# Performance work log

Hardware: AMD Instinct MI355X
Metric: run time of the kernel (lower is better)

## Reference

```python
import jax, jax.numpy as jnp
import numpy as np

B, H, S, D = 8, 16, 1024, 64

def setup_inputs() -> dict:
    key = jax.random.key(0)
    k1, k2, k3, k4 = jax.random.split(key, 4)
    Q = jax.random.normal(k1, (B, H, S, D), dtype=jnp.float32)
    K = jax.random.normal(k2, (B, H, S, D), dtype=jnp.float32)
    V = jax.random.normal(k3, (B, H, S, D), dtype=jnp.float32)
    mask = jax.random.randint(k4, (B,), 0, 2).astype(jnp.bool_)
    return {"Q": Q, "K": K, "V": V, "mask": mask}

def reference(Q, K, V, mask):
    # scores: [B,H,S,S]
    scores = jnp.einsum('bhqd,bhkd->bhqk', Q, K)
    # per-batch-element mask broadcast over heads and both seq dims
    scores = jnp.where(mask[:, None, None, None], jnp.float32(-1e9), scores)
    # NOTE: original divides by sqrt(d) AFTER masking, so masked value is -1e9/sqrt(d)
    inv_sqrt_d = jnp.float32(1.0 / np.sqrt(Q.shape[-1]))
    attn = jax.nn.softmax(scores * inv_sqrt_d, axis=-1)
    return jnp.einsum('bhqk,bhkd->bhqd', attn, V)
```

## Files before the change

### kernel.cpp

```cpp
#include <hip/hip_runtime.h>
#include <hip/hip_bf16.h>

typedef __bf16 bf16;
typedef __bf16 bf16x4 __attribute__((ext_vector_type(4)));
typedef __bf16 bf16x8 __attribute__((ext_vector_type(8)));
typedef float  f32x16 __attribute__((ext_vector_type(16)));

#define S_  1024
#define D_  64
#define BQ  256
#define BK  64
#define KT  (S_/BK)
#define QT  (S_/BQ)
#define LD  72

#define ZERO16 {0.f,0.f,0.f,0.f,0.f,0.f,0.f,0.f,0.f,0.f,0.f,0.f,0.f,0.f,0.f,0.f}

__global__ __launch_bounds__(256, 2)
void fa_fwd(const float* __restrict__ Q, const float* __restrict__ K,
            const float* __restrict__ V, const int* __restrict__ mask,
            float* __restrict__ O)
{
    __shared__ bf16 ks[2][BK][LD];
    __shared__ bf16 vt[2][D_][LD];

    const int tid  = threadIdx.x;
    const int lane = tid & 63;
    const int w    = tid >> 6;
    const int l32  = lane & 31;
    const int hi   = lane >> 5;
    const int bid  = blockIdx.x;

    int um[8] = { mask[0] == 0, mask[1] == 0, mask[2] == 0, mask[3] == 0,
                  mask[4] == 0, mask[5] == 0, mask[6] == 0, mask[7] == 0 };
    int U = 0;
    #pragma unroll
    for (int i = 0; i < 8; ++i) U += um[i];
    const int nHeavy = 64 * U;
    const int nLight = 16 * (8 - U);

    int bh, qtile;
    bool light;
    if (bid < nHeavy) {
        const int xcd = bid & 7;
        const int r   = bid >> 3;
        qtile = r & 3;
        const int g   = r >> 2;
        const int bh_rank = (g << 3) | xcd;
        const int ub   = bh_rank >> 4;
        const int head = bh_rank & 15;
        int b = 0, cnt = 0;
        #pragma unroll
        for (int i = 0; i < 8; ++i) { if (um[i]) { if (cnt == ub) b = i; ++cnt; } }
        bh = b * 16 + head;
        light = false;
    } else if (bid < nHeavy + nLight) {
        const int lid    = bid - nHeavy;
        const int m_rank = lid >> 4;
        const int head   = lid & 15;
        int b = 0, cnt = 0;
        #pragma unroll
        for (int i = 0; i < 8; ++i) { if (!um[i]) { if (cnt == m_rank) b = i; ++cnt; } }
        bh = b * 16 + head;
        qtile = 0;
        light = true;
    } else {
        return;
    }

    const size_t base = (size_t)bh * (S_ * D_);

    if (light) {
        const float4* gvl = (const float4*)(V + base);
        float4*       gol = (float4*)(O + base);
        const int d4 = tid & 15;
        const int rg = tid >> 4;
        float4 acc = {0.f, 0.f, 0.f, 0.f};
        #pragma unroll 4
        for (int r = 0; r < 64; ++r) {
            float4 v = gvl[(rg * 64 + r) * 16 + d4];
            acc.x += v.x; acc.y += v.y; acc.z += v.z; acc.w += v.w;
        }
        float4 (*red)[16] = (float4(*)[16])&ks[0][0][0];
        red[rg][d4] = acc;
        __syncthreads();
        if (tid < 16) {
            float4 s = red[0][tid];
            #pragma unroll
            for (int g = 1; g < 16; ++g) {
                float4 t = red[g][tid];
                s.x += t.x; s.y += t.y; s.z += t.z; s.w += t.w;
            }
            const float sc = 1.0f / 1024.0f;
            s.x *= sc; s.y *= sc; s.z *= sc; s.w *= sc;
            red[0][tid] = s;
        }
        __syncthreads();
        float4 mv = red[0][d4];
        #pragma unroll 4
        for (int k = 0; k < 64; ++k)
            gol[(rg + 16 * k) * 16 + d4] = mv;
        return;
    }

    const int qW = qtile * BQ + w * 64;
    const float qscale = 0.1803368801111204f;

    const int vkq = (tid >> 2) & 15;
    const int vkp = (vkq & 12) | ((vkq & 1) << 1) | ((vkq >> 1) & 1);
    const int vc4 = (tid & 3) + 4 * w;
    const float4* gk = (const float4*)(K + base);
    const float4* gv = (const float4*)(V + base);

    float4 kr[4], vr[4];
    #pragma unroll
    for (int it = 0; it < 4; ++it) kr[it] = gk[it * 256 + tid];
    #pragma unroll
    for (int r = 0; r < 4; ++r)    vr[r]  = gv[(vkq * 4 + r) * 16 + vc4];

    bf16x8 qf[2][4];
    #pragma unroll
    for (int nt = 0; nt < 2; ++nt) {
        const float* qp = Q + base + (size_t)(qW + nt * 32 + l32) * D_ + hi * 8;
        #pragma unroll
        for (int kc = 0; kc < 4; ++kc) {
            float4 a = *(const float4*)(qp + kc * 16);
            float4 c = *(const float4*)(qp + kc * 16 + 4);
            bf16x8 f;
            f[0] = (bf16)(a.x * qscale); f[1] = (bf16)(a.y * qscale);
            f[2] = (bf16)(a.z * qscale); f[3] = (bf16)(a.w * qscale);
            f[4] = (bf16)(c.x * qscale); f[5] = (bf16)(c.y * qscale);
            f[6] = (bf16)(c.z * qscale); f[7] = (bf16)(c.w * qscale);
            qf[nt][kc] = f;
        }
    }

    f32x16 o[2][2];
    #pragma unroll
    for (int dm = 0; dm < 2; ++dm)
        #pragma unroll
        for (int nt = 0; nt < 2; ++nt) o[dm][nt] = (f32x16)ZERO16;
    float lsum[2] = {0.f, 0.f};

    auto mkpf = [&](const f32x16& sv, bf16x8& fA, bf16x8& fB, float& ls) {
        bf16x8 a, c;
        #pragma unroll
        for (int i = 0; i < 8; ++i) {
            float e0 = __builtin_amdgcn_exp2f(sv[i]);
            float e1 = __builtin_amdgcn_exp2f(sv[8 + i]);
            ls += e0 + e1;
            a[i] = (bf16)e0;
            c[i] = (bf16)e1;
        }
        fA = a; fB = c;
    };

    for (int kt = 0; kt < KT; ++kt) {
        bf16 (*ksb)[LD] = ks[kt & 1];
        bf16 (*vtb)[LD] = vt[kt & 1];

        #pragma unroll
        for (int it = 0; it < 4; ++it) {
            int i = it * 256 + tid;
            int row = i >> 4, c4 = i & 15;
            bf16x4 hk = {(bf16)kr[it].x, (bf16)kr[it].y, (bf16)kr[it].z, (bf16)kr[it].w};
            *(bf16x4*)&ksb[row][c4 * 4] = hk;
        }
        {
            bf16x4 t0 = {(bf16)vr[0].x, (bf16)vr[1].x, (bf16)vr[2].x, (bf16)vr[3].x};
            bf16x4 t1 = {(bf16)vr[0].y, (bf16)vr[1].y, (bf16)vr[2].y, (bf16)vr[3].y};
            bf16x4 t2 = {(bf16)vr[0].z, (bf16)vr[1].z, (bf16)vr[2].z, (bf16)vr[3].z};
            bf16x4 t3 = {(bf16)vr[0].w, (bf16)vr[1].w, (bf16)vr[2].w, (bf16)vr[3].w};
            *(bf16x4*)&vtb[vc4 * 4 + 0][vkp * 4] = t0;
            *(bf16x4*)&vtb[vc4 * 4 + 1][vkp * 4] = t1;
            *(bf16x4*)&vtb[vc4 * 4 + 2][vkp * 4] = t2;
            *(bf16x4*)&vtb[vc4 * 4 + 3][vkp * 4] = t3;
        }

        __syncthreads();

        {
            int ktn = (kt + 1 < KT) ? (kt + 1) : kt;
            #pragma unroll
            for (int it = 0; it < 4; ++it) kr[it] = gk[ktn * 1024 + it * 256 + tid];
            #pragma unroll
            for (int r = 0; r < 4; ++r)    vr[r]  = gv[ktn * 1024 + (vkq * 4 + r) * 16 + vc4];
        }

        f32x16 s00 = ZERO16, s01 = ZERO16, s10 = ZERO16, s11 = ZERO16;
        #pragma unroll
        for (int kc = 0; kc < 4; ++kc) {
            bf16x8 k0 = *(const bf16x8*)&ksb[l32][kc * 16 + hi * 8];
            bf16x8 k1 = *(const bf16x8*)&ksb[32 + l32][kc * 16 + hi * 8];
            s00 = __builtin_amdgcn_mfma_f32_32x32x16_bf16(k0, qf[0][kc], s00, 0, 0, 0);
            s01 = __builtin_amdgcn_mfma_f32_32x32x16_bf16(k0, qf[1][kc], s01, 0, 0, 0);
            s10 = __builtin_amdgcn_mfma_f32_32x32x16_bf16(k1, qf[0][kc], s10, 0, 0, 0);
            s11 = __builtin_amdgcn_mfma_f32_32x32x16_bf16(k1, qf[1][kc], s11, 0, 0, 0);
        }

        bf16x8 pf[4][2];
        mkpf(s00, pf[0][0], pf[1][0], lsum[0]);
        mkpf(s01, pf[0][1], pf[1][1], lsum[1]);
        mkpf(s10, pf[2][0], pf[3][0], lsum[0]);
        mkpf(s11, pf[2][1], pf[3][1], lsum[1]);

        #pragma unroll
        for (int kc = 0; kc < 4; ++kc) {
            bf16x8 v0 = *(const bf16x8*)&vtb[l32][kc * 16 + hi * 8];
            bf16x8 v1 = *(const bf16x8*)&vtb[32 + l32][kc * 16 + hi * 8];
            o[0][0] = __builtin_amdgcn_mfma_f32_32x32x16_bf16(v0, pf[kc][0], o[0][0], 0, 0, 0);
            o[0][1] = __builtin_amdgcn_mfma_f32_32x32x16_bf16(v0, pf[kc][1], o[0][1], 0, 0, 0);
            o[1][0] = __builtin_amdgcn_mfma_f32_32x32x16_bf16(v1, pf[kc][0], o[1][0], 0, 0, 0);
            o[1][1] = __builtin_amdgcn_mfma_f32_32x32x16_bf16(v1, pf[kc][1], o[1][1], 0, 0, 0);
        }
    }

    #pragma unroll
    for (int nt = 0; nt < 2; ++nt) {
        float lv = lsum[nt] + __shfl_xor(lsum[nt], 32);
        float inv = 1.0f / lv;
        float* op = O + base + (size_t)(qW + nt * 32 + l32) * D_ + hi * 4;
        #pragma unroll
        for (int g = 0; g < 4; ++g) {
            float4 a = { o[0][nt][g * 4 + 0] * inv, o[0][nt][g * 4 + 1] * inv,
                         o[0][nt][g * 4 + 2] * inv, o[0][nt][g * 4 + 3] * inv };
            *(float4*)(op + g * 8) = a;
            float4 c = { o[1][nt][g * 4 + 0] * inv, o[1][nt][g * 4 + 1] * inv,
                         o[1][nt][g * 4 + 2] * inv, o[1][nt][g * 4 + 3] * inv };
            *(float4*)(op + 32 + g * 8) = c;
        }
    }
}

extern "C" void kernel_launch(void* const* d_in, const int* in_sizes, int n_in,
                              void* d_out, int out_size, void* d_ws, size_t ws_size,
                              hipStream_t stream)
{
    const float* Q    = (const float*)d_in[0];
    const float* K    = (const float*)d_in[1];
    const float* V    = (const float*)d_in[2];
    const int*   mask = (const int*)d_in[3];
    float*       O    = (float*)d_out;

    dim3 grid(8 * 16 * QT);
    fa_fwd<<<grid, 256, 0, stream>>>(Q, K, V, mask, O);
}
```

Before: 142.1 us.

## Software-pipeline QK and PV halves across key tiles with triple-buffered LDS

Splits each key tile's QK^T and exp/PV work into two 32-row halves and interleaves them across iterations, so the exp of one half overlaps MFMA work from the other half and the previous tile. LDS K/V buffers go from double to triple so the previous tile's V stays valid while the next tile is staged. The aim is to hide the exp2 and conversion latency behind matrix-core work. In exchange it uses more shared memory, which may reduce occupancy, and keeps more score accumulators live, which raises register pressure.

```diff
diff --git a/kernel.cpp b/kernel.cpp
--- a/kernel.cpp
+++ b/kernel.cpp
@@ -21,8 +21,8 @@
             const float* __restrict__ V, const int* __restrict__ mask,
             float* __restrict__ O)
 {
-    __shared__ bf16 ks[2][BK][LD];
-    __shared__ bf16 vt[2][D_][LD];
+    __shared__ bf16 ks[3][BK][LD];
+    __shared__ bf16 vt[3][D_][LD];
 
     const int tid  = threadIdx.x;
     const int lane = tid & 63;
@@ -142,6 +142,42 @@
         for (int nt = 0; nt < 2; ++nt) o[dm][nt] = (f32x16)ZERO16;
     float lsum[2] = {0.f, 0.f};
 
+    auto stage_to = [&](int bsel) {
+        bf16 (*ksb)[LD] = ks[bsel];
+        bf16 (*vtb)[LD] = vt[bsel];
+        #pragma unroll
+        for (int it = 0; it < 4; ++it) {
+            int i = it * 256 + tid;
+            int row = i >> 4, c4 = i & 15;
+            bf16x4 hk = {(bf16)kr[it].x, (bf16)kr[it].y, (bf16)kr[it].z, (bf16)kr[it].w};
+            *(bf16x4*)&ksb[row][c4 * 4] = hk;
+        }
+        bf16x4 t0 = {(bf16)vr[0].x, (bf16)vr[1].x, (bf16)vr[2].x, (bf16)vr[3].x};
+        bf16x4 t1 = {(bf16)vr[0].y, (bf16)vr[1].y, (bf16)vr[2].y, (bf16)vr[3].y};
+        bf16x4 t2 = {(bf16)vr[0].z, (bf16)vr[1].z, (bf16)vr[2].z, (bf16)vr[3].z};
+        bf16x4 t3 = {(bf16)vr[0].w, (bf16)vr[1].w, (bf16)vr[2].w, (bf16)vr[3].w};
+        *(bf16x4*)&vtb[vc4 * 4 + 0][vkp * 4] = t0;
+        *(bf16x4*)&vtb[vc4 * 4 + 1][vkp * 4] = t1;
+        *(bf16x4*)&vtb[vc4 * 4 + 2][vkp * 4] = t2;
+        *(bf16x4*)&vtb[vc4 * 4 + 3][vkp * 4] = t3;
+    };
+    auto prefetch_t = [&](int t) {
+        #pragma unroll
+        for (int it = 0; it < 4; ++it) kr[it] = gk[t * 1024 + it * 256 + tid];
+        #pragma unroll
+        for (int r = 0; r < 4; ++r)    vr[r]  = gv[t * 1024 + (vkq * 4 + r) * 16 + vc4];
+    };
+
+    auto qk_half = [&](int bsel, int rowoff, f32x16& s_0, f32x16& s_1) {
+        bf16 (*ksb)[LD] = ks[bsel];
+        #pragma unroll
+        for (int kc = 0; kc < 4; ++kc) {
+            bf16x8 kf = *(const bf16x8*)&ksb[rowoff + l32][kc * 16 + hi * 8];
+            s_0 = __builtin_amdgcn_mfma_f32_32x32x16_bf16(kf, qf[0][kc], s_0, 0, 0, 0);
+            s_1 = __builtin_amdgcn_mfma_f32_32x32x16_bf16(kf, qf[1][kc], s_1, 0, 0, 0);
+        }
+    };
+
     auto mkpf = [&](const f32x16& sv, bf16x8& fA, bf16x8& fB, float& ls) {
         bf16x8 a, c;
         #pragma unroll
@@ -155,65 +191,50 @@
         fA = a; fB = c;
     };
 
-    for (int kt = 0; kt < KT; ++kt) {
-        bf16 (*ksb)[LD] = ks[kt & 1];
-        bf16 (*vtb)[LD] = vt[kt & 1];
-
-        #pragma unroll
-        for (int it = 0; it < 4; ++it) {
-            int i = it * 256 + tid;
-            int row = i >> 4, c4 = i & 15;
-            bf16x4 hk = {(bf16)kr[it].x, (bf16)kr[it].y, (bf16)kr[it].z, (bf16)kr[it].w};
-            *(bf16x4*)&ksb[row][c4 * 4] = hk;
-        }
-        {
-            bf16x4 t0 = {(bf16)vr[0].x, (bf16)vr[1].x, (bf16)vr[2].x, (bf16)vr[3].x};
-            bf16x4 t1 = {(bf16)vr[0].y, (bf16)vr[1].y, (bf16)vr[2].y, (bf16)vr[3].y};
-            bf16x4 t2 = {(bf16)vr[0].z, (bf16)vr[1].z, (bf16)vr[2].z, (bf16)vr[3].z};
-            bf16x4 t3 = {(bf16)vr[0].w, (bf16)vr[1].w, (bf16)vr[2].w, (bf16)vr[3].w};
-            *(bf16x4*)&vtb[vc4 * 4 + 0][vkp * 4] = t0;
-            *(bf16x4*)&vtb[vc4 * 4 + 1][vkp * 4] = t1;
-            *(bf16x4*)&vtb[vc4 * 4 + 2][vkp * 4] = t2;
-            *(bf16x4*)&vtb[vc4 * 4 + 3][vkp * 4] = t3;
-        }
-
+    auto exp_pv_half = [&](const f32x16& s_0, const f32x16& s_1, int bsel, int kc0) {
+        bf16x8 a0, a1, b0, b1;
+        mkpf(s_0, a0, b0, lsum[0]);
+        mkpf(s_1, a1, b1, lsum[1]);
+        bf16 (*vtb)[LD] = vt[bsel];
+        bf16x8 v0 = *(const bf16x8*)&vtb[l32][kc0 * 16 + hi * 8];
+        bf16x8 v1 = *(const bf16x8*)&vtb[32 + l32][kc0 * 16 + hi * 8];
+        o[0][0] = __builtin_amdgcn_mfma_f32_32x32x16_bf16(v0, a0, o[0][0], 0, 0, 0);
+        o[0][1] = __builtin_amdgcn_mfma_f32_32x32x16_bf16(v0, a1, o[0][1], 0, 0, 0);
+        o[1][0] = __builtin_amdgcn_mfma_f32_32x32x16_bf16(v1, a0, o[1][0], 0, 0, 0);
+        o[1][1] = __builtin_amdgcn_mfma_f32_32x32x16_bf16(v1, a1, o[1][1], 0, 0, 0);
+        bf16x8 w0 = *(const bf16x8*)&vtb[l32][(kc0 + 1) * 16 + hi * 8];
+        bf16x8 w1 = *(const bf16x8*)&vtb[32 + l32][(kc0 + 1) * 16 + hi * 8];
+        o[0][0] = __builtin_amdgcn_mfma_f32_32x32x16_bf16(w0, b0, o[0][0], 0, 0, 0);
+        o[0][1] = __builtin_amdgcn_mfma_f32_32x32x16_bf16(w0, b1, o[0][1], 0, 0, 0);
+        o[1][0] = __builtin_amdgcn_mfma_f32_32x32x16_bf16(w1, b0, o[1][0], 0, 0, 0);
+        o[1][1] = __builtin_amdgcn_mfma_f32_32x32x16_bf16(w1, b1, o[1][1], 0, 0, 0);
+    };
+
+    f32x16 sA0, sA1, sB0, sB1;
+
+    stage_to(0);
+    __syncthreads();
+    prefetch_t(1);
+    sA0 = (f32x16)ZERO16; sA1 = (f32x16)ZERO16;
+    qk_half(0, 0,  sA0, sA1);
+    sB0 = (f32x16)ZERO16; sB1 = (f32x16)ZERO16;
+    qk_half(0, 32, sB0, sB1);
+    exp_pv_half(sA0, sA1, 0, 0);
+
+    int bs = 1, bp = 0;
+    for (int kt = 1; kt < KT; ++kt) {
+        stage_to(bs);
         __syncthreads();
-
-        {
-            int ktn = (kt + 1 < KT) ? (kt + 1) : kt;
-            #pragma unroll
-            for (int it = 0; it < 4; ++it) kr[it] = gk[ktn * 1024 + it * 256 + tid];
-            #pragma unroll
-            for (int r = 0; r < 4; ++r)    vr[r]  = gv[ktn * 1024 + (vkq * 4 + r) * 16 + vc4];
-        }
-
-        f32x16 s00 = ZERO16, s01 = ZERO16, s10 = ZERO16, s11 = ZERO16;
-        #pragma unroll
-        for (int kc = 0; kc < 4; ++kc) {
-            bf16x8 k0 = *(const bf16x8*)&ksb[l32][kc * 16 + hi * 8];
-            bf16x8 k1 = *(const bf16x8*)&ksb[32 + l32][kc * 16 + hi * 8];
-            s00 = __builtin_amdgcn_mfma_f32_32x32x16_bf16(k0, qf[0][kc], s00, 0, 0, 0);
-            s01 = __builtin_amdgcn_mfma_f32_32x32x16_bf16(k0, qf[1][kc], s01, 0, 0, 0);
-            s10 = __builtin_amdgcn_mfma_f32_32x32x16_bf16(k1, qf[0][kc], s10, 0, 0, 0);
-            s11 = __builtin_amdgcn_mfma_f32_32x32x16_bf16(k1, qf[1][kc], s11, 0, 0, 0);
-        }
-
-        bf16x8 pf[4][2];
-        mkpf(s00, pf[0][0], pf[1][0], lsum[0]);
-        mkpf(s01, pf[0][1], pf[1][1], lsum[1]);
-        mkpf(s10, pf[2][0], pf[3][0], lsum[0]);
-        mkpf(s11, pf[2][1], pf[3][1], lsum[1]);
-
-        #pragma unroll
-        for (int kc = 0; kc < 4; ++kc) {
-            bf16x8 v0 = *(const bf16x8*)&vtb[l32][kc * 16 + hi * 8];
-            bf16x8 v1 = *(const bf16x8*)&vtb[32 + l32][kc * 16 + hi * 8];
-            o[0][0] = __builtin_amdgcn_mfma_f32_32x32x16_bf16(v0, pf[kc][0], o[0][0], 0, 0, 0);
-            o[0][1] = __builtin_amdgcn_mfma_f32_32x32x16_bf16(v0, pf[kc][1], o[0][1], 0, 0, 0);
-            o[1][0] = __builtin_amdgcn_mfma_f32_32x32x16_bf16(v1, pf[kc][0], o[1][0], 0, 0, 0);
-            o[1][1] = __builtin_amdgcn_mfma_f32_32x32x16_bf16(v1, pf[kc][1], o[1][1], 0, 0, 0);
-        }
-    }
+        prefetch_t((kt + 1 < KT) ? (kt + 1) : kt);
+        sA0 = (f32x16)ZERO16; sA1 = (f32x16)ZERO16;
+        qk_half(bs, 0, sA0, sA1);
+        exp_pv_half(sB0, sB1, bp, 2);
+        sB0 = (f32x16)ZERO16; sB1 = (f32x16)ZERO16;
+        qk_half(bs, 32, sB0, sB1);
+        exp_pv_half(sA0, sA1, bs, 0);
+        bp = bs; bs = (bs == 2) ? 0 : bs + 1;
+    }
+    exp_pv_half(sB0, sB1, bp, 2);
 
     #pragma unroll
     for (int nt = 0; nt < 2; ++nt) {
```

New measurement: 145.3 us. 1.02x slower.

## Split block into producer and consumer wavefronts for K/V staging

Applied to the files above, without the earlier changes.

The block grows to 512 threads. Four new producer wavefronts load K/V from global memory, convert them to bf16 and stage them into double-buffered LDS, while the original four wavefronts only run the MFMA attention loop. The aim is to take global-load latency and conversion work off the compute wavefronts. The cost is a larger block, with launch bounds of 512x2 that squeeze the register budget per thread, which may cause spills in the consumer path. The light mean path is re-indexed for 512 threads.

```diff
diff --git a/kernel.cpp b/kernel.cpp
--- a/kernel.cpp
+++ b/kernel.cpp
@@ -16,7 +16,7 @@
 
 #define ZERO16 {0.f,0.f,0.f,0.f,0.f,0.f,0.f,0.f,0.f,0.f,0.f,0.f,0.f,0.f,0.f,0.f}
 
-__global__ __launch_bounds__(256, 2)
+__global__ __launch_bounds__(512, 2)
 void fa_fwd(const float* __restrict__ Q, const float* __restrict__ K,
             const float* __restrict__ V, const int* __restrict__ mask,
             float* __restrict__ O)
@@ -77,8 +77,8 @@
         const int rg = tid >> 4;
         float4 acc = {0.f, 0.f, 0.f, 0.f};
         #pragma unroll 4
-        for (int r = 0; r < 64; ++r) {
-            float4 v = gvl[(rg * 64 + r) * 16 + d4];
+        for (int r = 0; r < 32; ++r) {
+            float4 v = gvl[(rg * 32 + r) * 16 + d4];
             acc.x += v.x; acc.y += v.y; acc.z += v.z; acc.w += v.w;
         }
         float4 (*red)[16] = (float4(*)[16])&ks[0][0][0];
@@ -87,7 +87,7 @@
         if (tid < 16) {
             float4 s = red[0][tid];
             #pragma unroll
-            for (int g = 1; g < 16; ++g) {
+            for (int g = 1; g < 32; ++g) {
                 float4 t = red[g][tid];
                 s.x += t.x; s.y += t.y; s.z += t.z; s.w += t.w;
             }
@@ -98,136 +98,151 @@
         __syncthreads();
         float4 mv = red[0][d4];
         #pragma unroll 4
-        for (int k = 0; k < 64; ++k)
-            gol[(rg + 16 * k) * 16 + d4] = mv;
+        for (int k = 0; k < 32; ++k)
+            gol[(rg + 32 * k) * 16 + d4] = mv;
         return;
     }
 
-    const int qW = qtile * BQ + w * 64;
+    const bool consumer = (w < 4);
     const float qscale = 0.1803368801111204f;
 
-    const int vkq = (tid >> 2) & 15;
-    const int vkp = (vkq & 12) | ((vkq & 1) << 1) | ((vkq >> 1) & 1);
-    const int vc4 = (tid & 3) + 4 * w;
-    const float4* gk = (const float4*)(K + base);
-    const float4* gv = (const float4*)(V + base);
-
-    float4 kr[4], vr[4];
-    #pragma unroll
-    for (int it = 0; it < 4; ++it) kr[it] = gk[it * 256 + tid];
-    #pragma unroll
-    for (int r = 0; r < 4; ++r)    vr[r]  = gv[(vkq * 4 + r) * 16 + vc4];
-
-    bf16x8 qf[2][4];
-    #pragma unroll
-    for (int nt = 0; nt < 2; ++nt) {
-        const float* qp = Q + base + (size_t)(qW + nt * 32 + l32) * D_ + hi * 8;
-        #pragma unroll
-        for (int kc = 0; kc < 4; ++kc) {
-            float4 a = *(const float4*)(qp + kc * 16);
-            float4 c = *(const float4*)(qp + kc * 16 + 4);
-            bf16x8 f;
-            f[0] = (bf16)(a.x * qscale); f[1] = (bf16)(a.y * qscale);
-            f[2] = (bf16)(a.z * qscale); f[3] = (bf16)(a.w * qscale);
-            f[4] = (bf16)(c.x * qscale); f[5] = (bf16)(c.y * qscale);
-            f[6] = (bf16)(c.z * qscale); f[7] = (bf16)(c.w * qscale);
-            qf[nt][kc] = f;
-        }
-    }
-
-    f32x16 o[2][2];
-    #pragma unroll
-    for (int dm = 0; dm < 2; ++dm)
-        #pragma unroll
-        for (int nt = 0; nt < 2; ++nt) o[dm][nt] = (f32x16)ZERO16;
-    float lsum[2] = {0.f, 0.f};
-
-    auto mkpf = [&](const f32x16& sv, bf16x8& fA, bf16x8& fB, float& ls) {
-        bf16x8 a, c;
-        #pragma unroll
-        for (int i = 0; i < 8; ++i) {
-            float e0 = __builtin_amdgcn_exp2f(sv[i]);
-            float e1 = __builtin_amdgcn_exp2f(sv[8 + i]);
-            ls += e0 + e1;
-            a[i] = (bf16)e0;
-            c[i] = (bf16)e1;
-        }
-        fA = a; fB = c;
-    };
-
-    for (int kt = 0; kt < KT; ++kt) {
-        bf16 (*ksb)[LD] = ks[kt & 1];
-        bf16 (*vtb)[LD] = vt[kt & 1];
-
-        #pragma unroll
-        for (int it = 0; it < 4; ++it) {
-            int i = it * 256 + tid;
-            int row = i >> 4, c4 = i & 15;
-            bf16x4 hk = {(bf16)kr[it].x, (bf16)kr[it].y, (bf16)kr[it].z, (bf16)kr[it].w};
-            *(bf16x4*)&ksb[row][c4 * 4] = hk;
-        }
-        {
+    if (consumer) {
+        const int qW = qtile * BQ + w * 64;
+
+        bf16x8 qf[2][4];
+        #pragma unroll
+        for (int nt = 0; nt < 2; ++nt) {
+            const float* qp = Q + base + (size_t)(qW + nt * 32 + l32) * D_ + hi * 8;
+            #pragma unroll
+            for (int kc = 0; kc < 4; ++kc) {
+                float4 a = *(const float4*)(qp + kc * 16);
+                float4 c = *(const float4*)(qp + kc * 16 + 4);
+                bf16x8 f;
+                f[0] = (bf16)(a.x * qscale); f[1] = (bf16)(a.y * qscale);
+                f[2] = (bf16)(a.z * qscale); f[3] = (bf16)(a.w * qscale);
+                f[4] = (bf16)(c.x * qscale); f[5] = (bf16)(c.y * qscale);
+                f[6] = (bf16)(c.z * qscale); f[7] = (bf16)(c.w * qscale);
+                qf[nt][kc] = f;
+            }
+        }
+
+        f32x16 o[2][2];
+        #pragma unroll
+        for (int dm = 0; dm < 2; ++dm)
+            #pragma unroll
+            for (int nt = 0; nt < 2; ++nt) o[dm][nt] = (f32x16)ZERO16;
+        float lsum[2] = {0.f, 0.f};
+
+        auto mkpf = [&](const f32x16& sv, bf16x8& fA, bf16x8& fB, float& ls) {
+            bf16x8 a, c;
+            #pragma unroll
+            for (int i = 0; i < 8; ++i) {
+                float e0 = __builtin_amdgcn_exp2f(sv[i]);
+                float e1 = __builtin_amdgcn_exp2f(sv[8 + i]);
+                ls += e0 + e1;
+                a[i] = (bf16)e0;
+                c[i] = (bf16)e1;
+            }
+            fA = a; fB = c;
+        };
+
+        __syncthreads();
+
+        for (int kt = 0; kt < KT; ++kt) {
+            bf16 (*ksb)[LD] = ks[kt & 1];
+            bf16 (*vtb)[LD] = vt[kt & 1];
+
+            f32x16 s00 = ZERO16, s01 = ZERO16, s10 = ZERO16, s11 = ZERO16;
+            #pragma unroll
+            for (int kc = 0; kc < 4; ++kc) {
+                bf16x8 k0 = *(const bf16x8*)&ksb[l32][kc * 16 + hi * 8];
+                bf16x8 k1 = *(const bf16x8*)&ksb[32 + l32][kc * 16 + hi * 8];
+                s00 = __builtin_amdgcn_mfma_f32_32x32x16_bf16(k0, qf[0][kc], s00, 0, 0, 0);
+                s01 = __builtin_amdgcn_mfma_f32_32x32x16_bf16(k0, qf[1][kc], s01, 0, 0, 0);
+                s10 = __builtin_amdgcn_mfma_f32_32x32x16_bf16(k1, qf[0][kc], s10, 0, 0, 0);
+                s11 = __builtin_amdgcn_mfma_f32_32x32x16_bf16(k1, qf[1][kc], s11, 0, 0, 0);
+            }
+
+            bf16x8 pf[4][2];
+            mkpf(s00, pf[0][0], pf[1][0], lsum[0]);
+            mkpf(s01, pf[0][1], pf[1][1], lsum[1]);
+            mkpf(s10, pf[2][0], pf[3][0], lsum[0]);
+            mkpf(s11, pf[2][1], pf[3][1], lsum[1]);
+
+            #pragma unroll
+            for (int kc = 0; kc < 4; ++kc) {
+                bf16x8 v0 = *(const bf16x8*)&vtb[l32][kc * 16 + hi * 8];
+                bf16x8 v1 = *(const bf16x8*)&vtb[32 + l32][kc * 16 + hi * 8];
+                o[0][0] = __builtin_amdgcn_mfma_f32_32x32x16_bf16(v0, pf[kc][0], o[0][0], 0, 0, 0);
+                o[0][1] = __builtin_amdgcn_mfma_f32_32x32x16_bf16(v0, pf[kc][1], o[0][1], 0, 0, 0);
+                o[1][0] = __builtin_amdgcn_mfma_f32_32x32x16_bf16(v1, pf[kc][0], o[1][0], 0, 0, 0);
+                o[1][1] = __builtin_amdgcn_mfma_f32_32x32x16_bf16(v1, pf[kc][1], o[1][1], 0, 0, 0);
+            }
+
+            __syncthreads();
+        }
+
+        #pragma unroll
+        for (int nt = 0; nt < 2; ++nt) {
+            float lv = lsum[nt] + __shfl_xor(lsum[nt], 32);
+            float inv = 1.0f / lv;
+            float* op = O + base + (size_t)(qW + nt * 32 + l32) * D_ + hi * 4;
+            #pragma unroll
+            for (int g = 0; g < 4; ++g) {
+                float4 a = { o[0][nt][g * 4 + 0] * inv, o[0][nt][g * 4 + 1] * inv,
+                             o[0][nt][g * 4 + 2] * inv, o[0][nt][g * 4 + 3] * inv };
+                *(float4*)(op + g * 8) = a;
+                float4 c = { o[1][nt][g * 4 + 0] * inv, o[1][nt][g * 4 + 1] * inv,
+                             o[1][nt][g * 4 + 2] * inv, o[1][nt][g * 4 + 3] * inv };
+                *(float4*)(op + 32 + g * 8) = c;
+            }
+        }
+    } else {
+        const int t2  = tid - 256;
+        const int vkq = (t2 >> 2) & 15;
+        const int vkp = (vkq & 12) | ((vkq & 1) << 1) | ((vkq >> 1) & 1);
+        const int vc4 = (t2 & 3) + 4 * ((t2 >> 6) & 3);
+        const float4* gk = (const float4*)(K + base);
+        const float4* gv = (const float4*)(V + base);
+
+        float4 kr[4], vr[4];
+        auto prefetch_t = [&](int t) {
+            #pragma unroll
+            for (int it = 0; it < 4; ++it) kr[it] = gk[t * 1024 + it * 256 + t2];
+            #pragma unroll
+            for (int r = 0; r < 4; ++r)    vr[r]  = gv[t * 1024 + (vkq * 4 + r) * 16 + vc4];
+        };
+        auto stage_to = [&](int bsel) {
+            bf16 (*ksb)[LD] = ks[bsel];
+            bf16 (*vtb)[LD] = vt[bsel];
+            #pragma unroll
+            for (int it = 0; it < 4; ++it) {
+                int i = it * 256 + t2;
+                int row = i >> 4, c4 = i & 15;
+                bf16x4 hk = {(bf16)kr[it].x, (bf16)kr[it].y, (bf16)kr[it].z, (bf16)kr[it].w};
+                *(bf16x4*)&ksb[row][c4 * 4] = hk;
+            }
             bf16x4 t0 = {(bf16)vr[0].x, (bf16)vr[1].x, (bf16)vr[2].x, (bf16)vr[3].x};
             bf16x4 t1 = {(bf16)vr[0].y, (bf16)vr[1].y, (bf16)vr[2].y, (bf16)vr[3].y};
-            bf16x4 t2 = {(bf16)vr[0].z, (bf16)vr[1].z, (bf16)vr[2].z, (bf16)vr[3].z};
+            bf16x4 t2v = {(bf16)vr[0].z, (bf16)vr[1].z, (bf16)vr[2].z, (bf16)vr[3].z};
             bf16x4 t3 = {(bf16)vr[0].w, (bf16)vr[1].w, (bf16)vr[2].w, (bf16)vr[3].w};
             *(bf16x4*)&vtb[vc4 * 4 + 0][vkp * 4] = t0;
             *(bf16x4*)&vtb[vc4 * 4 + 1][vkp * 4] = t1;
-            *(bf16x4*)&vtb[vc4 * 4 + 2][vkp * 4] = t2;
+            *(bf16x4*)&vtb[vc4 * 4 + 2][vkp * 4] = t2v;
             *(bf16x4*)&vtb[vc4 * 4 + 3][vkp * 4] = t3;
-        }
-
-        __syncthreads();
-
-        {
-            int ktn = (kt + 1 < KT) ? (kt + 1) : kt;
-            #pragma unroll
-            for (int it = 0; it < 4; ++it) kr[it] = gk[ktn * 1024 + it * 256 + tid];
-            #pragma unroll
-            for (int r = 0; r < 4; ++r)    vr[r]  = gv[ktn * 1024 + (vkq * 4 + r) * 16 + vc4];
-        }
-
-        f32x16 s00 = ZERO16, s01 = ZERO16, s10 = ZERO16, s11 = ZERO16;
-        #pragma unroll
-        for (int kc = 0; kc < 4; ++kc) {
-            bf16x8 k0 = *(const bf16x8*)&ksb[l32][kc * 16 + hi * 8];
-            bf16x8 k1 = *(const bf16x8*)&ksb[32 + l32][kc * 16 + hi * 8];
-            s00 = __builtin_amdgcn_mfma_f32_32x32x16_bf16(k0, qf[0][kc], s00, 0, 0, 0);
-            s01 = __builtin_amdgcn_mfma_f32_32x32x16_bf16(k0, qf[1][kc], s01, 0, 0, 0);
-            s10 = __builtin_amdgcn_mfma_f32_32x32x16_bf16(k1, qf[0][kc], s10, 0, 0, 0);
-            s11 = __builtin_amdgcn_mfma_f32_32x32x16_bf16(k1, qf[1][kc], s11, 0, 0, 0);
-        }
-
-        bf16x8 pf[4][2];
-        mkpf(s00, pf[0][0], pf[1][0], lsum[0]);
-        mkpf(s01, pf[0][1], pf[1][1], lsum[1]);
-        mkpf(s10, pf[2][0], pf[3][0], lsum[0]);
-        mkpf(s11, pf[2][1], pf[3][1], lsum[1]);
-
-        #pragma unroll
-        for (int kc = 0; kc < 4; ++kc) {
-            bf16x8 v0 = *(const bf16x8*)&vtb[l32][kc * 16 + hi * 8];
-            bf16x8 v1 = *(const bf16x8*)&vtb[32 + l32][kc * 16 + hi * 8];
-            o[0][0] = __builtin_amdgcn_mfma_f32_32x32x16_bf16(v0, pf[kc][0], o[0][0], 0, 0, 0);
-            o[0][1] = __builtin_amdgcn_mfma_f32_32x32x16_bf16(v0, pf[kc][1], o[0][1], 0, 0, 0);
-            o[1][0] = __builtin_amdgcn_mfma_f32_32x32x16_bf16(v1, pf[kc][0], o[1][0], 0, 0, 0);
-            o[1][1] = __builtin_amdgcn_mfma_f32_32x32x16_bf16(v1, pf[kc][1], o[1][1], 0, 0, 0);
-        }
-    }
-
-    #pragma unroll
-    for (int nt = 0; nt < 2; ++nt) {
-        float lv = lsum[nt] + __shfl_xor(lsum[nt], 32);
-        float inv = 1.0f / lv;
-        float* op = O + base + (size_t)(qW + nt * 32 + l32) * D_ + hi * 4;
-        #pragma unroll
-        for (int g = 0; g < 4; ++g) {
-            float4 a = { o[0][nt][g * 4 + 0] * inv, o[0][nt][g * 4 + 1] * inv,
-                         o[0][nt][g * 4 + 2] * inv, o[0][nt][g * 4 + 3] * inv };
-            *(float4*)(op + g * 8) = a;
-            float4 c = { o[1][nt][g * 4 + 0] * inv, o[1][nt][g * 4 + 1] * inv,
-                         o[1][nt][g * 4 + 2] * inv, o[1][nt][g * 4 + 3] * inv };
-            *(float4*)(op + 32 + g * 8) = c;
+        };
+
+        prefetch_t(0);
+        stage_to(0);
+        prefetch_t(1);
+        __syncthreads();
+
+        for (int kt = 0; kt < KT; ++kt) {
+            if (kt + 1 < KT) {
+                stage_to((kt + 1) & 1);
+                if (kt + 2 < KT) prefetch_t(kt + 2);
+            }
+            __syncthreads();
         }
     }
 }
@@ -243,5 +258,5 @@
     float*       O    = (float*)d_out;
 
     dim3 grid(8 * 16 * QT);
-    fa_fwd<<<grid, 256, 0, stream>>>(Q, K, V, mask, O);
+    fa_fwd<<<grid, 512, 0, stream>>>(Q, K, V, mask, O);
 }
```

Result: faster. 133.8 us (-5.9%).
